# Kernel tuning notes

Hardware: AMD Instinct MI355X
Metric: run time of the kernel (lower is better)

Reference implementation:

```python
import jax, jax.numpy as jnp
import numpy as np

EPS = 1e-12


def t5_layer_norm(x, w):
    # RMS norm without mean subtraction (T5 style)
    var = jnp.mean(x * x, axis=-1, keepdims=True)
    return w * (x * jax.lax.rsqrt(var + EPS))


def gether(h, a_simi, t_simi, adj):
    # h: [B,S,S,D]; a_simi/t_simi: [B,S]; adj: [B,S,S]
    diag = jnp.einsum('bssd->bsd', h)                 # h[b,l,l,:]
    h_adj = jnp.einsum('bld,blk->blkd', diag, adj)    # diag broadcast by adjacency
    h_y = h * t_simi[:, None, :, None]                # t_simi varies along axis 2
    h_x = h * a_simi[:, :, None, None]                # a_simi varies along axis 1
    h_left = jnp.pad(h_y, ((0, 0), (0, 0), (1, 0), (0, 0)))[:, :, :-1, :]
    h_right = jnp.pad(h_y, ((0, 0), (0, 0), (0, 1), (0, 0)))[:, :, 1:, :]
    h_up = jnp.pad(h_x, ((0, 0), (1, 0), (0, 0), (0, 0)))[:, :-1, :, :]
    h_down = jnp.pad(h_x, ((0, 0), (0, 1), (0, 0), (0, 0)))[:, 1:, :, :]
    return h + h_adj + h_left + h_right + h_up + h_down


def setup_inputs() -> dict:
    key = jax.random.key(0)
    ks = jax.random.split(key, 10)
    B, S, D_in, D_out = 8, 96, 768, 256
    table = jax.random.normal(ks[0], (B, S, S, D_in), dtype=jnp.float32)
    a_simi = jax.random.uniform(ks[1], (B, S), dtype=jnp.float32)
    t_simi = jax.random.uniform(ks[2], (B, S), dtype=jnp.float32)
    adj_matrix = jax.random.uniform(ks[3], (B, S, S), dtype=jnp.float32)
    s1 = 1.0 / np.sqrt(D_in)
    W1 = jax.random.uniform(ks[4], (D_in, D_in), jnp.float32, -s1, s1)
    b1 = jax.random.uniform(ks[5], (D_in,), jnp.float32, -s1, s1)
    g1 = jnp.ones((D_in,), jnp.float32)
    W2 = jax.random.uniform(ks[6], (D_in, D_out), jnp.float32, -s1, s1)
    b2 = jax.random.uniform(ks[7], (D_out,), jnp.float32, -s1, s1)
    g2 = jnp.ones((D_out,), jnp.float32)
    return {"table": table, "a_simi": a_simi, "t_simi": t_simi,
            "adj_matrix": adj_matrix, "W1": W1, "b1": b1, "g1": g1,
            "W2": W2, "b2": b2, "g2": g2}


def reference(table, a_simi, t_simi, adj_matrix, W1, b1, g1, W2, b2, g2):
    h0 = table
    h1 = gether(h0, a_simi, t_simi, adj_matrix)
    h1 = jax.nn.relu(t5_layer_norm((h1 + h0) @ W1 + b1, g1))
    h2 = gether(h1, a_simi, t_simi, adj_matrix)
    h2 = jax.nn.relu(t5_layer_norm((h2 + h1) @ W2 + b2, g2))
    return h2
```

## Files before the change

### kernel.cpp

```cpp
#include <hip/hip_runtime.h>

typedef __bf16 bf16;
typedef __bf16 bf16x4 __attribute__((ext_vector_type(4)));
typedef __bf16 bf16x8 __attribute__((ext_vector_type(8)));
typedef float f32x4 __attribute__((ext_vector_type(4)));
typedef float floatx4 __attribute__((ext_vector_type(4)));

#define S 96
#define DIN 768
#define DOUT 256
#define MROWS 73728

__device__ static inline void async16(const bf16* g, bf16* l) {
    __builtin_amdgcn_global_load_lds(
        (const __attribute__((address_space(1))) void*)g,
        (__attribute__((address_space(3))) void*)l,
        16, 0, 0);
}

__global__ __launch_bounds__(256) void k_gether1(
    const float* __restrict__ H, const float* __restrict__ Asim,
    const float* __restrict__ Tsim, const float* __restrict__ Adj,
    bf16* __restrict__ X)
{
    __shared__ float adjs[S];
    __shared__ float ts[S];
    __shared__ float diagf[DIN];
    int bx = blockIdx.x;
    bx = (bx & 7) * (gridDim.x >> 3) + (bx >> 3);
    int b = bx / S, l = bx % S;
    int tid = threadIdx.x;
    long row0 = (long)(b * S + l) * S;
    if (tid < S) {
        adjs[tid] = Adj[(b * S + l) * S + tid];
        ts[tid]   = Tsim[b * S + tid];
    }
    for (int i = tid; i < DIN / 4; i += 256)
        *(f32x4*)&diagf[i * 4] = *(const f32x4*)&H[(row0 + l) * DIN + i * 4];
    float a_up = (l > 0)     ? Asim[b * S + l - 1] : 0.f;
    float a_dn = (l < S - 1) ? Asim[b * S + l + 1] : 0.f;
    long du = (l > 0)     ? -(long)S * DIN : 0;
    long dd = (l < S - 1) ?  (long)S * DIN : 0;
    __syncthreads();

    int lane = tid & 63, wv = tid >> 6;
    int k0 = blockIdx.y * (S / 2);
    for (int k = k0 + wv; k < k0 + S / 2; k += 4) {
        float tl = (k > 0)     ? ts[k - 1] : 0.f;
        float tr = (k < S - 1) ? ts[k + 1] : 0.f;
        long  dl = (k > 0)     ? -(long)DIN : 0;
        long  dr = (k < S - 1) ?  (long)DIN : 0;
        float aj = adjs[k];
        const float* hrow = H + (row0 + k) * DIN;
        bf16* xrow = X + (row0 + k) * DIN;
#pragma unroll
        for (int c = 0; c < 3; ++c) {
            int col = (lane + c * 64) * 4;
            const float* hc = hrow + col;
            f32x4 vc = *(const f32x4*)hc;
            f32x4 vl = *(const f32x4*)(hc + dl);
            f32x4 vr = *(const f32x4*)(hc + dr);
            f32x4 vu = *(const f32x4*)(hc + du);
            f32x4 vd = *(const f32x4*)(hc + dd);
            bf16x4 o;
#pragma unroll
            for (int j = 0; j < 4; ++j) {
                float v = 2.f * vc[j] + aj * diagf[col + j]
                        + tl * vl[j] + tr * vr[j]
                        + a_up * vu[j] + a_dn * vd[j];
                o[j] = (bf16)v;
            }
            *(bf16x4*)&xrow[col] = o;
        }
    }
}

__global__ __launch_bounds__(256) void k_gether2(
    const bf16* __restrict__ Y, const float* __restrict__ INV,
    const float* __restrict__ G1, const float* __restrict__ Asim,
    const float* __restrict__ Tsim, const float* __restrict__ Adj,
    bf16* __restrict__ X)
{
    __shared__ float adjs[S];
    __shared__ float ts[S];
    __shared__ float diagf[DIN];
    __shared__ float g1s[DIN];
    int bx = blockIdx.x;
    bx = (bx & 7) * (gridDim.x >> 3) + (bx >> 3);
    int b = bx / S, l = bx % S;
    int tid = threadIdx.x;
    long row0 = (long)(b * S + l) * S;
    for (int i = tid; i < DIN; i += 256) g1s[i] = G1[i];
    __syncthreads();
    if (tid < S) {
        adjs[tid] = Adj[(b * S + l) * S + tid];
        ts[tid]   = Tsim[b * S + tid];
        float iv = INV[row0 + l];
        bf16x8 yv = *(const bf16x8*)&Y[(row0 + l) * DIN + tid * 8];
#pragma unroll
        for (int j = 0; j < 8; ++j) {
            float v = g1s[tid * 8 + j] * (float)yv[j] * iv;
            diagf[tid * 8 + j] = v > 0.f ? v : 0.f;
        }
    }
    float a_up = (l > 0)     ? Asim[b * S + l - 1] : 0.f;
    float a_dn = (l < S - 1) ? Asim[b * S + l + 1] : 0.f;
    long du = (l > 0)     ? -(long)S * DIN : 0;
    long dd = (l < S - 1) ?  (long)S * DIN : 0;
    int ou = (l > 0) ? -S : 0;
    int od = (l < S - 1) ? S : 0;
    __syncthreads();

    int lane = tid & 63, wv = tid >> 6;
    int k0 = blockIdx.y * (S / 2);
    for (int k = k0 + wv; k < k0 + S / 2; k += 4) {
        float tl = (k > 0)     ? ts[k - 1] : 0.f;
        float tr = (k < S - 1) ? ts[k + 1] : 0.f;
        int   ol = (k > 0)     ? -1 : 0;
        int   orr = (k < S - 1) ? 1 : 0;
        float aj = adjs[k];
        float ivc = INV[row0 + k];
        float ivl = INV[row0 + k + ol];
        float ivr = INV[row0 + k + orr];
        float ivu = INV[row0 + k + ou];
        float ivd = INV[row0 + k + od];
        const bf16* yrow = Y + (row0 + k) * DIN;
        bf16* xrow = X + (row0 + k) * DIN;
#pragma unroll
        for (int c = 0; c < 3; ++c) {
            int col = (lane + c * 64) * 4;
            const bf16* yc = yrow + col;
            bf16x4 vc = *(const bf16x4*)yc;
            bf16x4 vl = *(const bf16x4*)(yc + (long)ol * DIN);
            bf16x4 vr = *(const bf16x4*)(yc + (long)orr * DIN);
            bf16x4 vu = *(const bf16x4*)(yc + du);
            bf16x4 vd = *(const bf16x4*)(yc + dd);
            bf16x4 o;
#pragma unroll
            for (int j = 0; j < 4; ++j) {
                float g = g1s[col + j];
                float hc_ = g * (float)vc[j] * ivc; hc_ = hc_ > 0.f ? hc_ : 0.f;
                float hl_ = g * (float)vl[j] * ivl; hl_ = hl_ > 0.f ? hl_ : 0.f;
                float hr_ = g * (float)vr[j] * ivr; hr_ = hr_ > 0.f ? hr_ : 0.f;
                float hu_ = g * (float)vu[j] * ivu; hu_ = hu_ > 0.f ? hu_ : 0.f;
                float hd_ = g * (float)vd[j] * ivd; hd_ = hd_ > 0.f ? hd_ : 0.f;
                float v = 2.f * hc_ + aj * diagf[col + j]
                        + tl * hl_ + tr * hr_ + a_up * hu_ + a_dn * hd_;
                o[j] = (bf16)v;
            }
            *(bf16x4*)&xrow[col] = o;
        }
    }
}

__global__ __launch_bounds__(512, 2) void k_gemm1(
    const bf16* __restrict__ Xm, const bf16* __restrict__ WT,
    const float* __restrict__ bias, bf16* __restrict__ Y,
    float* __restrict__ ssq)
{
    constexpr int K = 768, N = 768;
    constexpr int NTILE = K / 64;
    __shared__ __align__(16) bf16 As[2][256 * 64];
    __shared__ __align__(16) bf16 Bs[2][256 * 64];
    int t = threadIdx.x;
    int wg = blockIdx.x;
    wg = (wg & 7) * (gridDim.x >> 3) + (wg >> 3);
    int colBase = (wg % 3) * 256;
    int rowBase = (wg / 3) * 256;
    int lane = t & 63, w = t >> 6;
    int quad = lane >> 4, l16 = lane & 15;
    int wr = w >> 2, wc = w & 3;

    floatx4 acc[8][4];
#pragma unroll
    for (int i = 0; i < 8; ++i)
#pragma unroll
        for (int j = 0; j < 4; ++j) acc[i][j] = (floatx4)0.f;

    int tr = t >> 3;
    int gc = (t & 7) ^ (tr & 7);
    const bf16* gA = Xm + (size_t)(rowBase + tr) * K + gc * 8;
    const bf16* gB = WT + (size_t)(colBase + tr) * K + gc * 8;
    int ldst = t * 8;

    auto stageA = [&](int b, int s, int kt) {
        async16(gA + (size_t)s * 64 * K + kt * 64, &As[b][s * 4096 + ldst]);
    };
    auto stageB = [&](int b, int s, int kt) {
        async16(gB + (size_t)s * 64 * K + kt * 64, &Bs[b][s * 4096 + ldst]);
    };

    stageB(0, 0, 0); stageB(0, 1, 0); stageB(0, 2, 0); stageB(0, 3, 0);
    stageA(0, 0, 0); stageA(0, 2, 0); stageA(0, 1, 0); stageA(0, 3, 0);
    asm volatile("s_waitcnt vmcnt(2)" ::: "memory");
    __builtin_amdgcn_s_barrier();

    int swz = l16 & 7;
    int cK0 = (quad ^ swz) * 8;
    int cK1 = ((quad + 4) ^ swz) * 8;

    for (int tt = 0; tt < NTILE; ++tt) {
        int cur = tt & 1;
        int nb = cur ^ 1;
        bool more = (tt + 1 < NTILE);
        const bf16* aB = &As[cur][(wr * 128 + l16) * 64];
        const bf16* bB = &Bs[cur][(wc * 64 + l16) * 64];
#pragma unroll
        for (int p = 0; p < 4; ++p) {
            const int ihalf = p & 1;
            const int co = (p >> 1) ? cK1 : cK0;
            bf16x8 af[4], bfr[4];
#pragma unroll
            for (int ii = 0; ii < 4; ++ii)
                af[ii] = *(const bf16x8*)(aB + (ihalf * 4 + ii) * 1024 + co);
#pragma unroll
            for (int j = 0; j < 4; ++j)
                bfr[j] = *(const bf16x8*)(bB + j * 1024 + co);
            if (more) {
                if (p == 0) { stageB(nb, 0, tt + 1); stageB(nb, 1, tt + 1); }
                if (p == 1) { stageB(nb, 2, tt + 1); stageB(nb, 3, tt + 1); }
                if (p == 2) { stageA(nb, 0, tt + 1); stageA(nb, 2, tt + 1); }
                if (p == 3) { stageA(nb, 1, tt + 1); stageA(nb, 3, tt + 1); }
            }
            __builtin_amdgcn_s_barrier();
            asm volatile("s_waitcnt lgkmcnt(0)" ::: "memory");
            __builtin_amdgcn_sched_barrier(0);
            __builtin_amdgcn_s_setprio(1);
#pragma unroll
            for (int ii = 0; ii < 4; ++ii)
#pragma unroll
                for (int j = 0; j < 4; ++j)
                    acc[ihalf * 4 + ii][j] = __builtin_amdgcn_mfma_f32_16x16x32_bf16(
                        af[ii], bfr[j], acc[ihalf * 4 + ii][j], 0, 0, 0);
            __builtin_amdgcn_s_setprio(0);
            if (p == 0) {
                if (more) asm volatile("s_waitcnt vmcnt(2)" ::: "memory");
                else      asm volatile("s_waitcnt vmcnt(0)" ::: "memory");
            }
            if (p == 3 && more) asm volatile("s_waitcnt vmcnt(2)" ::: "memory");
            __builtin_amdgcn_s_barrier();
        }
    }

    float bv[4];
#pragma unroll
    for (int j = 0; j < 4; ++j)
        bv[j] = bias[colBase + wc * 64 + j * 16 + l16];
#pragma unroll
    for (int i = 0; i < 8; ++i) {
#pragma unroll
        for (int r = 0; r < 4; ++r) {
            int row = rowBase + wr * 128 + i * 16 + quad * 4 + r;
            bf16* yp = Y + (size_t)row * N + colBase + wc * 64 + l16;
            float s = 0.f;
#pragma unroll
            for (int j = 0; j < 4; ++j) {
                float v = acc[i][j][r] + bv[j];
                s += v * v;
                yp[j * 16] = (bf16)v;
            }
            s += __shfl_xor(s, 1);
            s += __shfl_xor(s, 2);
            s += __shfl_xor(s, 4);
            s += __shfl_xor(s, 8);
            if (l16 == 0) atomicAdd(&ssq[row], s);
        }
    }
}

__global__ __launch_bounds__(256, 2) void k_gemm2f(
    const bf16* __restrict__ Xm, const bf16* __restrict__ WT,
    const float* __restrict__ bias, const float* __restrict__ G2,
    float* __restrict__ out)
{
    constexpr int K = 768, N = 256;
    constexpr int NT = K / 32;
    __shared__ __align__(16) bf16 As[3][128 * 32];
    __shared__ __align__(16) bf16 Bs[3][256 * 32];
    __shared__ float ssqs[2][128];
    int t = threadIdx.x;
    int rowBase = blockIdx.x * 128;
    int lane = t & 63, w = t >> 6;
    int quad = lane >> 4, l16 = lane & 15;
    int wr = w >> 1, wc = w & 1;

    floatx4 acc[4][8];
#pragma unroll
    for (int i = 0; i < 4; ++i)
#pragma unroll
        for (int j = 0; j < 8; ++j) acc[i][j] = (floatx4)0.f;

    int chunk = (t & 3) ^ ((t >> 3) & 3);
    const bf16* gA = Xm + (size_t)(rowBase + (t >> 2)) * K + chunk * 8;
    const bf16* gB = WT + (size_t)(t >> 2) * K + chunk * 8;
    int l8 = t * 8;

    auto stage = [&](int buf, int kk) {
        async16(gA + kk, &As[buf][l8]);
        async16(gA + kk + 64 * K, &As[buf][l8 + 2048]);
        async16(gB + kk, &Bs[buf][l8]);
        async16(gB + kk + 64 * K, &Bs[buf][l8 + 2048]);
        async16(gB + kk + 128 * K, &Bs[buf][l8 + 4096]);
        async16(gB + kk + 192 * K, &Bs[buf][l8 + 6144]);
    };

    stage(0, 0);
    stage(1, 32);
    for (int tt = 0; tt < NT; ++tt) {
        if (tt + 1 < NT) asm volatile("s_waitcnt vmcnt(6)" ::: "memory");
        else             asm volatile("s_waitcnt vmcnt(0)" ::: "memory");
        __builtin_amdgcn_s_barrier();
        int cur = tt % 3;
        bf16x8 af[4], bfr[8];
#pragma unroll
        for (int i = 0; i < 4; ++i) {
            int ra = wr * 64 + i * 16 + l16;
            af[i] = *(const bf16x8*)&As[cur][ra * 32 + (quad ^ ((ra >> 1) & 3)) * 8];
        }
#pragma unroll
        for (int j = 0; j < 8; ++j) {
            int rb = wc * 128 + j * 16 + l16;
            bfr[j] = *(const bf16x8*)&Bs[cur][rb * 32 + (quad ^ ((rb >> 1) & 3)) * 8];
        }
        if (tt + 2 < NT) stage((tt + 2) % 3, (tt + 2) * 32);
#pragma unroll
        for (int i = 0; i < 4; ++i)
#pragma unroll
            for (int j = 0; j < 8; ++j)
                acc[i][j] = __builtin_amdgcn_mfma_f32_16x16x32_bf16(
                    af[i], bfr[j], acc[i][j], 0, 0, 0);
    }

    float bv[8], gv[8];
#pragma unroll
    for (int j = 0; j < 8; ++j) {
        int col = wc * 128 + j * 16 + l16;
        bv[j] = bias[col];
        gv[j] = G2[col];
    }
#pragma unroll
    for (int i = 0; i < 4; ++i) {
#pragma unroll
        for (int r = 0; r < 4; ++r) {
            float s = 0.f;
#pragma unroll
            for (int j = 0; j < 8; ++j) {
                float v = acc[i][j][r] + bv[j];
                s += v * v;
            }
            s += __shfl_xor(s, 1);
            s += __shfl_xor(s, 2);
            s += __shfl_xor(s, 4);
            s += __shfl_xor(s, 8);
            if (l16 == 0)
                ssqs[wc][wr * 64 + i * 16 + quad * 4 + r] = s;
        }
    }
    __syncthreads();
#pragma unroll
    for (int i = 0; i < 4; ++i) {
#pragma unroll
        for (int r = 0; r < 4; ++r) {
            int lr = wr * 64 + i * 16 + quad * 4 + r;
            float inv = rsqrtf((ssqs[0][lr] + ssqs[1][lr]) * (1.f / N) + 1e-12f);
            float* op = out + (size_t)(rowBase + lr) * N + wc * 128 + l16;
#pragma unroll
            for (int j = 0; j < 8; ++j) {
                float v = (acc[i][j][r] + bv[j]) * gv[j] * inv;
                op[j * 16] = v > 0.f ? v : 0.f;
            }
        }
    }
}

__global__ __launch_bounds__(256) void k_invr(float* ssq, int n, float invD)
{
    int i = blockIdx.x * 256 + threadIdx.x;
    if (i < n) ssq[i] = rsqrtf(ssq[i] * invD + 1e-12f);
}

__global__ __launch_bounds__(256) void k_castT(
    const float* __restrict__ in, bf16* __restrict__ out, int R, int C)
{
    __shared__ float tile[32][33];
    int lx = threadIdx.x & 31, ly = threadIdx.x >> 5;
    int c0 = blockIdx.x * 32, r0 = blockIdx.y * 32;
#pragma unroll
    for (int k = 0; k < 4; ++k)
        tile[ly + 8 * k][lx] = in[(size_t)(r0 + ly + 8 * k) * C + c0 + lx];
    __syncthreads();
#pragma unroll
    for (int k = 0; k < 4; ++k)
        out[(size_t)(c0 + ly + 8 * k) * R + r0 + lx] = (bf16)tile[lx][ly + 8 * k];
}

extern "C" void kernel_launch(void* const* d_in, const int* in_sizes, int n_in,
                              void* d_out, int out_size, void* d_ws, size_t ws_size,
                              hipStream_t stream)
{
    const float* table = (const float*)d_in[0];
    const float* asim  = (const float*)d_in[1];
    const float* tsim  = (const float*)d_in[2];
    const float* adj   = (const float*)d_in[3];
    const float* W1    = (const float*)d_in[4];
    const float* b1    = (const float*)d_in[5];
    const float* g1    = (const float*)d_in[6];
    const float* W2    = (const float*)d_in[7];
    const float* b2    = (const float*)d_in[8];
    const float* g2    = (const float*)d_in[9];
    float* out = (float*)d_out;

    char* ws = (char*)d_ws;
    const size_t SZ_X = (size_t)MROWS * DIN * 2;
    bf16*  X    = (bf16*)ws;
    bf16*  Y1   = (bf16*)(ws + SZ_X);
    bf16*  W1T  = (bf16*)(ws + 2 * SZ_X);
    bf16*  W2T  = (bf16*)(ws + 2 * SZ_X + 1179648);
    float* ssq1 = (float*)(ws + 2 * SZ_X + 1179648 + 393216);

    hipMemsetAsync(ssq1, 0, (size_t)MROWS * 4, stream);
    k_castT<<<dim3(DIN / 32, DIN / 32), 256, 0, stream>>>(W1, W1T, DIN, DIN);
    k_castT<<<dim3(DOUT / 32, DIN / 32), 256, 0, stream>>>(W2, W2T, DIN, DOUT);

    k_gether1<<<dim3(8 * S, 2), 256, 0, stream>>>(table, asim, tsim, adj, X);
    k_gemm1<<<dim3((DIN / 256) * (MROWS / 256)), 512, 0, stream>>>(X, W1T, b1, Y1, ssq1);
    k_invr<<<MROWS / 256, 256, 0, stream>>>(ssq1, MROWS, 1.f / DIN);
    k_gether2<<<dim3(8 * S, 2), 256, 0, stream>>>(Y1, ssq1, g1, asim, tsim, adj, X);
    k_gemm2f<<<MROWS / 128, 256, 0, stream>>>(X, W2T, b2, g2, out);
}
```

Before: 637.6 us.

## Apply GEMMs before the linear gather stencil and fuse bias with RMS norm

The gather stencil is linear, so it commutes with right-multiplication by W. Each GEMM now runs first on the raw activations, and the stencil, bias, T5 RMS norm and ReLU are applied afterwards in one fused kernel per layer. The row norm is done with a wave-level shuffle reduction, which removes the atomic sum-of-squares accumulation, the memset and the separate rsqrt kernel. The second stencil now works on the 256-wide output instead of the 768-wide hidden state. In exchange it adds a full fp32-to-bf16 cast pass over the input table and a bf16 round trip for the GEMM2 output, and the pre-norm values are rounded to bf16 before the stencil.

Result: faster. 595.1 us (-6.7%).

```diff
diff --git a/kernel.cpp b/kernel.cpp
--- a/kernel.cpp
+++ b/kernel.cpp
@@ -18,145 +18,24 @@
         16, 0, 0);
 }
 
-__global__ __launch_bounds__(256) void k_gether1(
-    const float* __restrict__ H, const float* __restrict__ Asim,
-    const float* __restrict__ Tsim, const float* __restrict__ Adj,
-    bf16* __restrict__ X)
-{
-    __shared__ float adjs[S];
-    __shared__ float ts[S];
-    __shared__ float diagf[DIN];
-    int bx = blockIdx.x;
-    bx = (bx & 7) * (gridDim.x >> 3) + (bx >> 3);
-    int b = bx / S, l = bx % S;
-    int tid = threadIdx.x;
-    long row0 = (long)(b * S + l) * S;
-    if (tid < S) {
-        adjs[tid] = Adj[(b * S + l) * S + tid];
-        ts[tid]   = Tsim[b * S + tid];
-    }
-    for (int i = tid; i < DIN / 4; i += 256)
-        *(f32x4*)&diagf[i * 4] = *(const f32x4*)&H[(row0 + l) * DIN + i * 4];
-    float a_up = (l > 0)     ? Asim[b * S + l - 1] : 0.f;
-    float a_dn = (l < S - 1) ? Asim[b * S + l + 1] : 0.f;
-    long du = (l > 0)     ? -(long)S * DIN : 0;
-    long dd = (l < S - 1) ?  (long)S * DIN : 0;
-    __syncthreads();
-
-    int lane = tid & 63, wv = tid >> 6;
-    int k0 = blockIdx.y * (S / 2);
-    for (int k = k0 + wv; k < k0 + S / 2; k += 4) {
-        float tl = (k > 0)     ? ts[k - 1] : 0.f;
-        float tr = (k < S - 1) ? ts[k + 1] : 0.f;
-        long  dl = (k > 0)     ? -(long)DIN : 0;
-        long  dr = (k < S - 1) ?  (long)DIN : 0;
-        float aj = adjs[k];
-        const float* hrow = H + (row0 + k) * DIN;
-        bf16* xrow = X + (row0 + k) * DIN;
-#pragma unroll
-        for (int c = 0; c < 3; ++c) {
-            int col = (lane + c * 64) * 4;
-            const float* hc = hrow + col;
-            f32x4 vc = *(const f32x4*)hc;
-            f32x4 vl = *(const f32x4*)(hc + dl);
-            f32x4 vr = *(const f32x4*)(hc + dr);
-            f32x4 vu = *(const f32x4*)(hc + du);
-            f32x4 vd = *(const f32x4*)(hc + dd);
-            bf16x4 o;
-#pragma unroll
-            for (int j = 0; j < 4; ++j) {
-                float v = 2.f * vc[j] + aj * diagf[col + j]
-                        + tl * vl[j] + tr * vr[j]
-                        + a_up * vu[j] + a_dn * vd[j];
-                o[j] = (bf16)v;
-            }
-            *(bf16x4*)&xrow[col] = o;
-        }
-    }
-}
-
-__global__ __launch_bounds__(256) void k_gether2(
-    const bf16* __restrict__ Y, const float* __restrict__ INV,
-    const float* __restrict__ G1, const float* __restrict__ Asim,
-    const float* __restrict__ Tsim, const float* __restrict__ Adj,
-    bf16* __restrict__ X)
-{
-    __shared__ float adjs[S];
-    __shared__ float ts[S];
-    __shared__ float diagf[DIN];
-    __shared__ float g1s[DIN];
-    int bx = blockIdx.x;
-    bx = (bx & 7) * (gridDim.x >> 3) + (bx >> 3);
-    int b = bx / S, l = bx % S;
-    int tid = threadIdx.x;
-    long row0 = (long)(b * S + l) * S;
-    for (int i = tid; i < DIN; i += 256) g1s[i] = G1[i];
-    __syncthreads();
-    if (tid < S) {
-        adjs[tid] = Adj[(b * S + l) * S + tid];
-        ts[tid]   = Tsim[b * S + tid];
-        float iv = INV[row0 + l];
-        bf16x8 yv = *(const bf16x8*)&Y[(row0 + l) * DIN + tid * 8];
-#pragma unroll
-        for (int j = 0; j < 8; ++j) {
-            float v = g1s[tid * 8 + j] * (float)yv[j] * iv;
-            diagf[tid * 8 + j] = v > 0.f ? v : 0.f;
-        }
-    }
-    float a_up = (l > 0)     ? Asim[b * S + l - 1] : 0.f;
-    float a_dn = (l < S - 1) ? Asim[b * S + l + 1] : 0.f;
-    long du = (l > 0)     ? -(long)S * DIN : 0;
-    long dd = (l < S - 1) ?  (long)S * DIN : 0;
-    int ou = (l > 0) ? -S : 0;
-    int od = (l < S - 1) ? S : 0;
-    __syncthreads();
-
-    int lane = tid & 63, wv = tid >> 6;
-    int k0 = blockIdx.y * (S / 2);
-    for (int k = k0 + wv; k < k0 + S / 2; k += 4) {
-        float tl = (k > 0)     ? ts[k - 1] : 0.f;
-        float tr = (k < S - 1) ? ts[k + 1] : 0.f;
-        int   ol = (k > 0)     ? -1 : 0;
-        int   orr = (k < S - 1) ? 1 : 0;
-        float aj = adjs[k];
-        float ivc = INV[row0 + k];
-        float ivl = INV[row0 + k + ol];
-        float ivr = INV[row0 + k + orr];
-        float ivu = INV[row0 + k + ou];
-        float ivd = INV[row0 + k + od];
-        const bf16* yrow = Y + (row0 + k) * DIN;
-        bf16* xrow = X + (row0 + k) * DIN;
-#pragma unroll
-        for (int c = 0; c < 3; ++c) {
-            int col = (lane + c * 64) * 4;
-            const bf16* yc = yrow + col;
-            bf16x4 vc = *(const bf16x4*)yc;
-            bf16x4 vl = *(const bf16x4*)(yc + (long)ol * DIN);
-            bf16x4 vr = *(const bf16x4*)(yc + (long)orr * DIN);
-            bf16x4 vu = *(const bf16x4*)(yc + du);
-            bf16x4 vd = *(const bf16x4*)(yc + dd);
-            bf16x4 o;
-#pragma unroll
-            for (int j = 0; j < 4; ++j) {
-                float g = g1s[col + j];
-                float hc_ = g * (float)vc[j] * ivc; hc_ = hc_ > 0.f ? hc_ : 0.f;
-                float hl_ = g * (float)vl[j] * ivl; hl_ = hl_ > 0.f ? hl_ : 0.f;
-                float hr_ = g * (float)vr[j] * ivr; hr_ = hr_ > 0.f ? hr_ : 0.f;
-                float hu_ = g * (float)vu[j] * ivu; hu_ = hu_ > 0.f ? hu_ : 0.f;
-                float hd_ = g * (float)vd[j] * ivd; hd_ = hd_ > 0.f ? hd_ : 0.f;
-                float v = 2.f * hc_ + aj * diagf[col + j]
-                        + tl * hl_ + tr * hr_ + a_up * hu_ + a_dn * hd_;
-                o[j] = (bf16)v;
-            }
-            *(bf16x4*)&xrow[col] = o;
-        }
+__global__ __launch_bounds__(256) void k_cast(
+    const float* __restrict__ in, bf16* __restrict__ out, long n)
+{
+    long i = ((long)blockIdx.x * 256 + threadIdx.x) * 8;
+    long stride = (long)gridDim.x * 256 * 8;
+    for (; i < n; i += stride) {
+        f32x4 a = *(const f32x4*)&in[i];
+        f32x4 b = *(const f32x4*)&in[i + 4];
+        bf16x8 o;
+#pragma unroll
+        for (int j = 0; j < 4; ++j) { o[j] = (bf16)a[j]; o[4 + j] = (bf16)b[j]; }
+        *(bf16x8*)&out[i] = o;
     }
 }
 
 __global__ __launch_bounds__(512, 2) void k_gemm1(
     const bf16* __restrict__ Xm, const bf16* __restrict__ WT,
-    const float* __restrict__ bias, bf16* __restrict__ Y,
-    float* __restrict__ ssq)
+    bf16* __restrict__ Y)
 {
     constexpr int K = 768, N = 768;
     constexpr int NTILE = K / 64;
@@ -242,42 +121,109 @@
         }
     }
 
-    float bv[4];
-#pragma unroll
-    for (int j = 0; j < 4; ++j)
-        bv[j] = bias[colBase + wc * 64 + j * 16 + l16];
 #pragma unroll
     for (int i = 0; i < 8; ++i) {
 #pragma unroll
         for (int r = 0; r < 4; ++r) {
             int row = rowBase + wr * 128 + i * 16 + quad * 4 + r;
             bf16* yp = Y + (size_t)row * N + colBase + wc * 64 + l16;
-            float s = 0.f;
+#pragma unroll
+            for (int j = 0; j < 4; ++j)
+                yp[j * 16] = (bf16)acc[i][j][r];
+        }
+    }
+}
+
+__global__ __launch_bounds__(256) void k_gn1(
+    const bf16* __restrict__ P, const float* __restrict__ G1,
+    const float* __restrict__ B1, const float* __restrict__ Asim,
+    const float* __restrict__ Tsim, const float* __restrict__ Adj,
+    bf16* __restrict__ O)
+{
+    __shared__ float adjs[S];
+    __shared__ float ts[S];
+    __shared__ float diagf[DIN];
+    __shared__ float g1s[DIN];
+    __shared__ float b1s[DIN];
+    int bx = blockIdx.x;
+    bx = (bx & 7) * (gridDim.x >> 3) + (bx >> 3);
+    int b = bx / S, l = bx % S;
+    int tid = threadIdx.x;
+    long row0 = (long)(b * S + l) * S;
+    for (int i = tid; i < DIN; i += 256) { g1s[i] = G1[i]; b1s[i] = B1[i]; }
+    if (tid < S) {
+        adjs[tid] = Adj[(b * S + l) * S + tid];
+        ts[tid]   = Tsim[b * S + tid];
+        bf16x8 dv = *(const bf16x8*)&P[(row0 + l) * DIN + tid * 8];
+#pragma unroll
+        for (int j = 0; j < 8; ++j) diagf[tid * 8 + j] = (float)dv[j];
+    }
+    float a_up = (l > 0)     ? Asim[b * S + l - 1] : 0.f;
+    float a_dn = (l < S - 1) ? Asim[b * S + l + 1] : 0.f;
+    long du = (l > 0)     ? -(long)S * DIN : 0;
+    long dd = (l < S - 1) ?  (long)S * DIN : 0;
+    __syncthreads();
+
+    int lane = tid & 63, wv = tid >> 6;
+    int k0 = blockIdx.y * (S / 2);
+    for (int k = k0 + wv; k < k0 + S / 2; k += 4) {
+        float tl = (k > 0)     ? ts[k - 1] : 0.f;
+        float tr = (k < S - 1) ? ts[k + 1] : 0.f;
+        long  dl = (k > 0)     ? -(long)DIN : 0;
+        long  dr = (k < S - 1) ?  (long)DIN : 0;
+        float aj = adjs[k];
+        const bf16* prow = P + (row0 + k) * DIN;
+        bf16* orow = O + (row0 + k) * DIN;
+        float v[12];
+        float ss = 0.f;
+#pragma unroll
+        for (int c = 0; c < 3; ++c) {
+            int col = (lane + c * 64) * 4;
+            const bf16* pc = prow + col;
+            bf16x4 vc = *(const bf16x4*)pc;
+            bf16x4 vl = *(const bf16x4*)(pc + dl);
+            bf16x4 vr = *(const bf16x4*)(pc + dr);
+            bf16x4 vu = *(const bf16x4*)(pc + du);
+            bf16x4 vd = *(const bf16x4*)(pc + dd);
 #pragma unroll
             for (int j = 0; j < 4; ++j) {
-                float v = acc[i][j][r] + bv[j];
-                s += v * v;
-                yp[j * 16] = (bf16)v;
+                float x = 2.f * (float)vc[j] + aj * diagf[col + j]
+                        + tl * (float)vl[j] + tr * (float)vr[j]
+                        + a_up * (float)vu[j] + a_dn * (float)vd[j]
+                        + b1s[col + j];
+                v[c * 4 + j] = x;
+                ss += x * x;
             }
-            s += __shfl_xor(s, 1);
-            s += __shfl_xor(s, 2);
-            s += __shfl_xor(s, 4);
-            s += __shfl_xor(s, 8);
-            if (l16 == 0) atomicAdd(&ssq[row], s);
-        }
-    }
-}
-
-__global__ __launch_bounds__(256, 2) void k_gemm2f(
+        }
+        ss += __shfl_xor(ss, 1);
+        ss += __shfl_xor(ss, 2);
+        ss += __shfl_xor(ss, 4);
+        ss += __shfl_xor(ss, 8);
+        ss += __shfl_xor(ss, 16);
+        ss += __shfl_xor(ss, 32);
+        float inv = rsqrtf(ss * (1.f / DIN) + 1e-12f);
+#pragma unroll
+        for (int c = 0; c < 3; ++c) {
+            int col = (lane + c * 64) * 4;
+            bf16x4 o;
+#pragma unroll
+            for (int j = 0; j < 4; ++j) {
+                float y = v[c * 4 + j] * g1s[col + j] * inv;
+                o[j] = (bf16)(y > 0.f ? y : 0.f);
+            }
+            *(bf16x4*)&orow[col] = o;
+        }
+    }
+}
+
+__global__ __launch_bounds__(256, 2) void k_gemm2(
     const bf16* __restrict__ Xm, const bf16* __restrict__ WT,
-    const float* __restrict__ bias, const float* __restrict__ G2,
-    float* __restrict__ out)
+    bf16* __restrict__ Y)
 {
     constexpr int K = 768, N = 256;
     constexpr int NT = K / 32;
     __shared__ __align__(16) bf16 As[3][128 * 32];
     __shared__ __align__(16) bf16 Bs[3][256 * 32];
-    __shared__ float ssqs[2][128];
     int t = threadIdx.x;
     int rowBase = blockIdx.x * 128;
     int lane = t & 63, w = t >> 6;
@@ -331,52 +277,94 @@
                     af[i], bfr[j], acc[i][j], 0, 0, 0);
     }
 
-    float bv[8], gv[8];
-#pragma unroll
-    for (int j = 0; j < 8; ++j) {
-        int col = wc * 128 + j * 16 + l16;
-        bv[j] = bias[col];
-        gv[j] = G2[col];
-    }
 #pragma unroll
     for (int i = 0; i < 4; ++i) {
 #pragma unroll
         for (int r = 0; r < 4; ++r) {
-            float s = 0.f;
-#pragma unroll
-            for (int j = 0; j < 8; ++j) {
-                float v = acc[i][j][r] + bv[j];
-                s += v * v;
-            }
-            s += __shfl_xor(s, 1);
-            s += __shfl_xor(s, 2);
-            s += __shfl_xor(s, 4);
-            s += __shfl_xor(s, 8);
-            if (l16 == 0)
-                ssqs[wc][wr * 64 + i * 16 + quad * 4 + r] = s;
-        }
-    }
+            int row = rowBase + wr * 64 + i * 16 + quad * 4 + r;
+            bf16* yp = Y + (size_t)row * N + wc * 128 + l16;
+#pragma unroll
+            for (int j = 0; j < 8; ++j)
+                yp[j * 16] = (bf16)acc[i][j][r];
+        }
+    }
+}
+
+__global__ __launch_bounds__(256) void k_gn2(
+    const bf16* __restrict__ P, const float* __restrict__ G2,
+    const float* __restrict__ B2, const float* __restrict__ Asim,
+    const float* __restrict__ Tsim, const float* __restrict__ Adj,
+    float* __restrict__ O)
+{
+    __shared__ float adjs[S];
+    __shared__ float ts[S];
+    __shared__ float diagf[DOUT];
+    __shared__ float g2s[DOUT];
+    __shared__ float b2s[DOUT];
+    int bx = blockIdx.x;
+    bx = (bx & 7) * (gridDim.x >> 3) + (bx >> 3);
+    int b = bx / S, l = bx % S;
+    int tid = threadIdx.x;
+    long row0 = (long)(b * S + l) * S;
+    if (tid < DOUT) { g2s[tid] = G2[tid]; b2s[tid] = B2[tid]; }
+    if (tid < S) {
+        adjs[tid] = Adj[(b * S + l) * S + tid];
+        ts[tid]   = Tsim[b * S + tid];
+    }
+    if (tid < 32) {
+        bf16x8 dv = *(const bf16x8*)&P[(row0 + l) * DOUT + tid * 8];
+#pragma unroll
+        for (int j = 0; j < 8; ++j) diagf[tid * 8 + j] = (float)dv[j];
+    }
+    float a_up = (l > 0)     ? Asim[b * S + l - 1] : 0.f;
+    float a_dn = (l < S - 1) ? Asim[b * S + l + 1] : 0.f;
+    long du = (l > 0)     ? -(long)S * DOUT : 0;
+    long dd = (l < S - 1) ?  (long)S * DOUT : 0;
     __syncthreads();
-#pragma unroll
-    for (int i = 0; i < 4; ++i) {
-#pragma unroll
-        for (int r = 0; r < 4; ++r) {
-            int lr = wr * 64 + i * 16 + quad * 4 + r;
-            float inv = rsqrtf((ssqs[0][lr] + ssqs[1][lr]) * (1.f / N) + 1e-12f);
-            float* op = out + (size_t)(rowBase + lr) * N + wc * 128 + l16;
-#pragma unroll
-            for (int j = 0; j < 8; ++j) {
-                float v = (acc[i][j][r] + bv[j]) * gv[j] * inv;
-                op[j * 16] = v > 0.f ? v : 0.f;
-            }
-        }
-    }
-}
-
-__global__ __launch_bounds__(256) void k_invr(float* ssq, int n, float invD)
-{
-    int i = blockIdx.x * 256 + threadIdx.x;
-    if (i < n) ssq[i] = rsqrtf(ssq[i] * invD + 1e-12f);
+
+    int lane = tid & 63, wv = tid >> 6;
+    int k0 = blockIdx.y * (S / 2);
+    for (int k = k0 + wv; k < k0 + S / 2; k += 4) {
+        float tl = (k > 0)     ? ts[k - 1] : 0.f;
+        float tr = (k < S - 1) ? ts[k + 1] : 0.f;
+        long  dl = (k > 0)     ? -(long)DOUT : 0;
+        long  dr = (k < S - 1) ?  (long)DOUT : 0;
+        float aj = adjs[k];
+        const bf16* prow = P + (row0 + k) * DOUT;
+        float* orow = O + (row0 + k) * DOUT;
+        int col = lane * 4;
+        const bf16* pc = prow + col;
+        bf16x4 vc = *(const bf16x4*)pc;
+        bf16x4 vl = *(const bf16x4*)(pc + dl);
+        bf16x4 vr = *(const bf16x4*)(pc + dr);
+        bf16x4 vu = *(const bf16x4*)(pc + du);
+        bf16x4 vd = *(const bf16x4*)(pc + dd);
+        float v[4];
+        float ss = 0.f;
+#pragma unroll
+        for (int j = 0; j < 4; ++j) {
+            float x = 2.f * (float)vc[j] + aj * diagf[col + j]
+                    + tl * (float)vl[j] + tr * (float)vr[j]
+                    + a_up * (float)vu[j] + a_dn * (float)vd[j]
+                    + b2s[col + j];
+            v[j] = x;
+            ss += x * x;
+        }
+        ss += __shfl_xor(ss, 1);
+        ss += __shfl_xor(ss, 2);
+        ss += __shfl_xor(ss, 4);
+        ss += __shfl_xor(ss, 8);
+        ss += __shfl_xor(ss, 16);
+        ss += __shfl_xor(ss, 32);
+        float inv = rsqrtf(ss * (1.f / DOUT) + 1e-12f);
+        f32x4 o;
+#pragma unroll
+        for (int j = 0; j < 4; ++j) {
+            float y = v[j] * g2s[col + j] * inv;
+            o[j] = y > 0.f ? y : 0.f;
+        }
+        *(f32x4*)&orow[col] = o;
+    }
 }
 
 __global__ __launch_bounds__(256) void k_castT(
@@ -412,19 +400,17 @@
 
     char* ws = (char*)d_ws;
     const size_t SZ_X = (size_t)MROWS * DIN * 2;
-    bf16*  X    = (bf16*)ws;
-    bf16*  Y1   = (bf16*)(ws + SZ_X);
+    bf16*  A    = (bf16*)ws;
+    bf16*  Bb   = (bf16*)(ws + SZ_X);
     bf16*  W1T  = (bf16*)(ws + 2 * SZ_X);
     bf16*  W2T  = (bf16*)(ws + 2 * SZ_X + 1179648);
-    float* ssq1 = (float*)(ws + 2 * SZ_X + 1179648 + 393216);
-
-    hipMemsetAsync(ssq1, 0, (size_t)MROWS * 4, stream);
+
     k_castT<<<dim3(DIN / 32, DIN / 32), 256, 0, stream>>>(W1, W1T, DIN, DIN);
     k_castT<<<dim3(DOUT / 32, DIN / 32), 256, 0, stream>>>(W2, W2T, DIN, DOUT);
 
-    k_gether1<<<dim3(8 * S, 2), 256, 0, stream>>>(table, asim, tsim, adj, X);
-    k_gemm1<<<dim3((DIN / 256) * (MROWS / 256)), 512, 0, stream>>>(X, W1T, b1, Y1, ssq1);
-    k_invr<<<MROWS / 256, 256, 0, stream>>>(ssq1, MROWS, 1.f / DIN);
-    k_gether2<<<dim3(8 * S, 2), 256, 0, stream>>>(Y1, ssq1, g1, asim, tsim, adj, X);
-    k_gemm2f<<<MROWS / 128, 256, 0, stream>>>(X, W2T, b2, g2, out);
-}
+    k_cast<<<2048, 256, 0, stream>>>(table, A, (long)MROWS * DIN);
+    k_gemm1<<<dim3((DIN / 256) * (MROWS / 256)), 512, 0, stream>>>(A, W1T, Bb);
+    k_gn1<<<dim3(8 * S, 2), 256, 0, stream>>>(Bb, g1, b1, asim, tsim, adj, A);
+    k_gemm2<<<MROWS / 128, 256, 0, stream>>>(A, W2T, Bb);
+    k_gn2<<<dim3(8 * S, 2), 256, 0, stream>>>(Bb, g2, b2, asim, tsim, adj, out);
+}
```
